# Kernel optimization log

Hardware: AMD Instinct MI355X
Metric: run time of the kernel (lower is better)

## Reference

```python
import jax, jax.numpy as jnp
import numpy as np

B, S, H = 16, 1024, 1024  # S must equal H for the original bmm to type-check


def setup_inputs() -> dict:
    key = jax.random.key(0)
    k1, k2, k3, k4, k5 = jax.random.split(key, 5)
    ht = jax.random.normal(k1, (B, H), dtype=jnp.float32)
    encoder_out = jax.random.normal(k2, (B, S, H), dtype=jnp.float32)
    # nn.Linear(2H, H): weight [H, 2H], bias [H]
    W_attn = jax.random.normal(k3, (H, 2 * H), dtype=jnp.float32) / np.sqrt(2 * H)
    b_attn = jax.random.normal(k4, (H,), dtype=jnp.float32) * 0.01
    # nn.Linear(H, 1, bias=False): weight [1, H]  (computed in forward but its output is discarded)
    W_v = jax.random.normal(k5, (1, H), dtype=jnp.float32) / np.sqrt(H)
    return {"ht": ht, "encoder_out": encoder_out, "W_attn": W_attn, "b_attn": b_attn, "W_v": W_v}


def reference(ht, encoder_out, W_attn, b_attn, W_v):
    b, s, h = encoder_out.shape
    # ht.repeat(S,1,1).transpose(0,1) -> [B,S,H]
    ht_rep = jnp.broadcast_to(ht[:, None, :], (b, s, h))
    energy = jnp.concatenate([ht_rep, encoder_out], axis=2)          # [B,S,2H]
    energy = jnp.tanh(jnp.einsum('bsk,hk->bsh', energy, W_attn) + b_attn)  # [B,S,H]
    # v projection is computed in the original forward but not returned (dead output)
    _attention = jnp.einsum('bsh,oh->bso', energy, W_v)[..., 0]      # [B,S], unused
    # NOTE: softmax over dim=1 (the seq axis) of the full 3D energy, as in the original
    attention_weights = jax.nn.softmax(energy, axis=1)               # [B,S,H]
    # bmm([B,S,H],[B,S,H]) with S==H: contract weights' H axis vs encoder_out's S axis
    context = jnp.einsum('bsk,bkh->bsh', attention_weights, encoder_out)  # [B,S,H]
    return (context, attention_weights)
```

## Files before the change

kernel.cpp:

```cpp
#include <hip/hip_runtime.h>
#include <math.h>

#define Bn 16
#define Sn 1024
#define Hn 1024
static const size_t SH = (size_t)Sn * Hn;
static const size_t BSH = (size_t)Bn * Sn * Hn;

typedef __attribute__((ext_vector_type(8))) short short8;
typedef __attribute__((ext_vector_type(4))) float f32x4;

#define GLD16(gp, lp) __builtin_amdgcn_global_load_lds( \
    (const __attribute__((address_space(1))) void*)(gp), \
    (__attribute__((address_space(3))) void*)(lp), 16, 0, 0)

__device__ __forceinline__ short bfr(float f) {
  union { float f; unsigned u; } v; v.f = f;
  unsigned r = (v.u + 0x7FFFu + ((v.u >> 16) & 1u)) >> 16;
  return (short)r;
}
__device__ __forceinline__ float b2f(unsigned short u) {
  union { unsigned u; float f; } v; v.u = (unsigned)u << 16; return v.f;
}
__device__ __forceinline__ short8 cvt8(float4 x, float4 y) {
  short8 r;
  r[0] = bfr(x.x); r[1] = bfr(x.y); r[2] = bfr(x.z); r[3] = bfr(x.w);
  r[4] = bfr(y.x); r[5] = bfr(y.y); r[6] = bfr(y.z); r[7] = bfr(y.w);
  return r;
}

__device__ __forceinline__ int swz8(int row, int g) {
  return (g & ~7) | ((g & 7) ^ (row & 7));
}

__global__ __launch_bounds__(256) void fused_cvt_kernel(const float* __restrict__ enc,
                                                        short* __restrict__ enc_bf,
                                                        short* __restrict__ encT) {
  __shared__ float tile[64][65];
  const int b = blockIdx.z;
  const int s0 = blockIdx.y * 64, h0 = blockIdx.x * 64;
  const int t = threadIdx.x;
  const int tr = t >> 4, tc = t & 15;
  const float* src = enc + (size_t)b * SH;
#pragma unroll
  for (int i = 0; i < 4; ++i) {
    const int s = i * 16 + tr;
    const float4 v = *(const float4*)(src + (size_t)(s0 + s) * 1024 + h0 + tc * 4);
    tile[s][tc * 4 + 0] = v.x; tile[s][tc * 4 + 1] = v.y;
    tile[s][tc * 4 + 2] = v.z; tile[s][tc * 4 + 3] = v.w;
  }
  __syncthreads();
  {
    const int rloc = t >> 2;
    const int rg = b * 1024 + s0 + rloc;
#pragma unroll
    for (int jj = 0; jj < 2; ++jj) {
      const int jloc = (t & 3) * 2 + jj;
      const int slot = jloc ^ (rg & 7);
      const float4 x = *(const float4*)&tile[rloc][jloc * 8];
      const float4 y = *(const float4*)&tile[rloc][jloc * 8 + 4];
      *(short8*)(enc_bf + (size_t)rg * 1024 + h0 + slot * 8) = cvt8(x, y);
    }
  }
  {
    const int hr = t >> 2, cs = t & 3;
    const int h = h0 + hr;
#pragma unroll
    for (int blk = 0; blk < 2; ++blk) {
      const int sg = blk * 4 + cs;
      const int gl = (s0 >> 3) + sg;
      const int gst = swz8(h, gl);
      short8 pk;
#pragma unroll
      for (int j = 0; j < 8; ++j) pk[j] = bfr(tile[sg * 8 + j][hr]);
      *(short8*)(encT + (size_t)b * SH + (size_t)h * 1024 + gst * 8) = pk;
    }
  }
}

__global__ __launch_bounds__(256) void cvt_enc_kernel(const float* __restrict__ enc,
                                                      short* __restrict__ enc_bf) {
  const int g = blockIdx.x * 256 + threadIdx.x;
  const int row = g >> 7;
  const int cs = g & 127;
  const float4 x = *(const float4*)(enc + (size_t)row * 1024 + cs * 8);
  const float4 y = *(const float4*)(enc + (size_t)row * 1024 + cs * 8 + 4);
  *(short8*)(enc_bf + (size_t)row * 1024 + swz8(row, cs) * 8) = cvt8(x, y);
}

__global__ __launch_bounds__(256) void cvt_w2_kernel(const float* __restrict__ W_attn,
                                                     short* __restrict__ W2_bf) {
  const int g = blockIdx.x * 256 + threadIdx.x;
  const int h = g >> 7;
  const int cs = g & 127;
  const float4 x = *(const float4*)(W_attn + (size_t)h * 2048 + 1024 + cs * 8);
  const float4 y = *(const float4*)(W_attn + (size_t)h * 2048 + 1024 + cs * 8 + 4);
  *(short8*)(W2_bf + (size_t)h * 1024 + swz8(h, cs) * 8) = cvt8(x, y);
}

__global__ __launch_bounds__(256) void c1_kernel(const float* __restrict__ ht,
                                                 const float* __restrict__ W_attn,
                                                 const float* __restrict__ b_attn,
                                                 float* __restrict__ c1) {
  __shared__ float hts[16384];
  const int t = threadIdx.x;
#pragma unroll
  for (int i = 0; i < 16; ++i)
    *(float4*)&hts[i * 1024 + t * 4] = *(const float4*)&ht[i * 1024 + t * 4];
  __syncthreads();
  const int h = blockIdx.x * 4 + (t >> 6);
  const int lane = t & 63;
  const float* w = W_attn + (size_t)h * 2048;
  float s[16];
#pragma unroll
  for (int b = 0; b < 16; ++b) s[b] = 0.f;
  for (int k = lane; k < 1024; k += 64) {
    const float wv = w[k];
#pragma unroll
    for (int b = 0; b < 16; ++b) s[b] = fmaf(wv, hts[b * 1024 + k], s[b]);
  }
#pragma unroll
  for (int b = 0; b < 16; ++b) {
    float v = s[b];
#pragma unroll
    for (int off = 32; off; off >>= 1) v += __shfl_down(v, off, 64);
    if (lane == 0) c1[b * 1024 + h] = v + b_attn[h];
  }
}

__global__ __launch_bounds__(256) void energy_mfma5(const short* __restrict__ enc_bf,
                                                    const short* __restrict__ W2_bf,
                                                    const float* __restrict__ c1,
                                                    short* __restrict__ Xbf,
                                                    float* __restrict__ colsum) {
  __shared__ __align__(16) short SMEM[2 * 128 * 64];
  short* Ast = SMEM;
  short* Bst = SMEM + 128 * 64;
  const int flat = blockIdx.x + (blockIdx.y << 3) + (blockIdx.z << 6);
  const int swz = (flat & 7) * 128 + (flat >> 3);
  const int b = swz >> 6;
  const int row0 = ((swz >> 3) & 7) * 128;
  const int col0 = (swz & 7) * 128;
  const int t = threadIdx.x;
  const int l = t & 63;
  const int w = t >> 6;
  const int wr = w >> 1, wc = w & 1;
  const int fr = l & 15, kg = l >> 4;

  const short* Abase = enc_bf + (size_t)b * SH + (size_t)(row0 + w * 32 + (l >> 3)) * 1024 + (l & 7) * 8;
  const short* Bbase = W2_bf + (size_t)(col0 + w * 32 + (l >> 3)) * 1024 + (l & 7) * 8;
  short* Alds = Ast + w * 2048;
  short* Blds = Bst + w * 2048;

  f32x4 acc[4][4] = {};

  for (int k0 = 0; k0 < 1024; k0 += 64) {
#pragma unroll
    for (int j = 0; j < 4; ++j) {
      GLD16(Abase + k0 + j * 8 * 1024, Alds + j * 512);
      GLD16(Bbase + k0 + j * 8 * 1024, Blds + j * 512);
    }
    __syncthreads();
#pragma unroll
    for (int kk = 0; kk < 2; ++kk) {
      short8 af[4], bf4[4];
#pragma unroll
      for (int m = 0; m < 4; ++m) {
        const int r = wr * 64 + m * 16 + fr;
        af[m] = *(const short8*)&Ast[r * 64 + (((kk * 4 + kg) ^ (r & 7)) << 3)];
      }
#pragma unroll
      for (int n = 0; n < 4; ++n) {
        const int r = wc * 64 + n * 16 + fr;
        bf4[n] = *(const short8*)&Bst[r * 64 + (((kk * 4 + kg) ^ (r & 7)) << 3)];
      }
#pragma unroll
      for (int m = 0; m < 4; ++m)
#pragma unroll
        for (int n = 0; n < 4; ++n)
          acc[m][n] = __builtin_amdgcn_mfma_f32_16x16x32_bf16(af[m], bf4[n], acc[m][n], 0, 0, 0);
    }
    __syncthreads();
  }

  unsigned short* obuf = (unsigned short*)SMEM;
#pragma unroll
  for (int n = 0; n < 4; ++n) {
    const int col_loc = wc * 64 + n * 16 + fr;
    const float c1v = c1[b * 1024 + col0 + col_loc];
    float csum = 0.f;
#pragma unroll
    for (int m = 0; m < 4; ++m) {
      const int rbase = wr * 64 + m * 16 + kg * 4;
#pragma unroll
      for (int r = 0; r < 4; ++r) {
        const float x = acc[m][n][r] + c1v;
        const float e = __expf(2.f * x);
        const float X = __expf((e - 1.f) / (e + 1.f));
        csum += X;
        const int row = rbase + r;
        obuf[row * 128 + (col_loc ^ ((row & 7) << 3))] = (unsigned short)bfr(X);
      }
    }
    csum += __shfl_xor(csum, 16);
    csum += __shfl_xor(csum, 32);
    if (l < 16) atomicAdd(&colsum[b * 1024 + col0 + col_loc], csum);
  }
  __syncthreads();
  const int orow = t >> 1;
  short* gdst = Xbf + (size_t)b * SH + (size_t)(row0 + orow) * 1024 + col0;
#pragma unroll
  for (int j = 0; j < 8; ++j) {
    const int slot = (t & 1) * 8 + j;
    *(short8*)(gdst + slot * 8) = *(short8*)&obuf[orow * 128 + slot * 8];
  }
}

__global__ __launch_bounds__(256) void rcp_kernel(const float* __restrict__ cs,
                                                  float* __restrict__ ci) {
  const int i = blockIdx.x * 256 + threadIdx.x;
  ci[i] = 1.0f / cs[i];
}

__global__ __launch_bounds__(256) void scale_v1(short* __restrict__ Xbf,
                                                const float* __restrict__ colinv,
                                                float* __restrict__ aw) {
  const size_t gid = (size_t)blockIdx.x * 256 + threadIdx.x;
  const int rg = (int)(gid >> 7);
  const int ss = (int)(gid & 127);
  const int b = rg >> 10;
  const int gl = (ss & ~7) | ((ss & 7) ^ (rg & 7));
  const int h0 = gl * 8;
  short* p = Xbf + (size_t)rg * 1024 + ss * 8;
  const short8 v = *(const short8*)p;
  const float4 ci0 = *(const float4*)(colinv + (b << 10) + h0);
  const float4 ci1 = *(const float4*)(colinv + (b << 10) + h0 + 4);
  float f[8];
  f[0] = b2f((unsigned short)v[0]) * ci0.x; f[1] = b2f((unsigned short)v[1]) * ci0.y;
  f[2] = b2f((unsigned short)v[2]) * ci0.z; f[3] = b2f((unsigned short)v[3]) * ci0.w;
  f[4] = b2f((unsigned short)v[4]) * ci1.x; f[5] = b2f((unsigned short)v[5]) * ci1.y;
  f[6] = b2f((unsigned short)v[6]) * ci1.z; f[7] = b2f((unsigned short)v[7]) * ci1.w;
  float4 o0 = {f[0], f[1], f[2], f[3]};
  float4 o1 = {f[4], f[5], f[6], f[7]};
  *(float4*)(aw + (size_t)rg * 1024 + h0) = o0;
  *(float4*)(aw + (size_t)rg * 1024 + h0 + 4) = o1;
  short8 r;
#pragma unroll
  for (int j = 0; j < 8; ++j) r[j] = bfr(f[j]);
  *(short8*)p = r;
}

__global__ __launch_bounds__(256) void context_gld(const short* __restrict__ awbf,
                                                   const short* __restrict__ encT,
                                                   float* __restrict__ ctx) {
  __shared__ __align__(16) short Ast[128 * 64];
  __shared__ __align__(16) short Bst[128 * 64];
  const int flat = blockIdx.x + (blockIdx.y << 3) + (blockIdx.z << 6);
  const int swz = (flat & 7) * 128 + (flat >> 3);
  const int b = swz >> 6;
  const int row0 = ((swz >> 3) & 7) * 128;
  const int col0 = (swz & 7) * 128;
  const int t = threadIdx.x;
  const int l = t & 63;
  const int w = t >> 6;
  const int wr = w >> 1, wc = w & 1;
  const int fr = l & 15, kg = l >> 4;

  const short* Abase = awbf + (size_t)b * SH + (size_t)(row0 + w * 32 + (l >> 3)) * 1024 + (l & 7) * 8;
  const short* Bbase = encT + (size_t)b * SH + (size_t)(col0 + w * 32 + (l >> 3)) * 1024 + (l & 7) * 8;
  short* Alds = Ast + w * 2048;
  short* Blds = Bst + w * 2048;

  f32x4 acc[4][4] = {};

  for (int k0 = 0; k0 < 1024; k0 += 64) {
#pragma unroll
    for (int j = 0; j < 4; ++j) {
      GLD16(Abase + k0 + j * 8 * 1024, Alds + j * 512);
      GLD16(Bbase + k0 + j * 8 * 1024, Blds + j * 512);
    }
    __syncthreads();
#pragma unroll
    for (int kk = 0; kk < 2; ++kk) {
      short8 af[4], bf4[4];
#pragma unroll
      for (int m = 0; m < 4; ++m) {
        const int r = wr * 64 + m * 16 + fr;
        af[m] = *(const short8*)&Ast[r * 64 + (((kk * 4 + kg) ^ (r & 7)) << 3)];
      }
#pragma unroll
      for (int n = 0; n < 4; ++n) {
        const int r = wc * 64 + n * 16 + fr;
        bf4[n] = *(const short8*)&Bst[r * 64 + (((kk * 4 + kg) ^ (r & 7)) << 3)];
      }
#pragma unroll
      for (int m = 0; m < 4; ++m)
#pragma unroll
        for (int n = 0; n < 4; ++n)
          acc[m][n] = __builtin_amdgcn_mfma_f32_16x16x32_bf16(af[m], bf4[n], acc[m][n], 0, 0, 0);
    }
    __syncthreads();
  }

  float* Cb = ctx + (size_t)b * SH;
#pragma unroll
  for (int n = 0; n < 4; ++n) {
    const int col = col0 + wc * 64 + n * 16 + fr;
#pragma unroll
    for (int m = 0; m < 4; ++m) {
      const int r0 = row0 + wr * 64 + m * 16 + kg * 4;
#pragma unroll
      for (int r = 0; r < 4; ++r)
        Cb[(size_t)(r0 + r) * 1024 + col] = acc[m][n][r];
    }
  }
}

__global__ __launch_bounds__(256) void energy_mfma4(const short* __restrict__ enc_bf,
                                                    const short* __restrict__ W2_bf,
                                                    const float* __restrict__ c1,
                                                    float* __restrict__ X) {
  __shared__ __align__(16) short Ast[128 * 64];
  __shared__ __align__(16) short Bst[128 * 64];
  const int flat = blockIdx.x + (blockIdx.y << 3) + (blockIdx.z << 6);
  const int swz = (flat & 7) * 128 + (flat >> 3);
  const int b = swz >> 6;
  const int row0 = ((swz >> 3) & 7) * 128;
  const int col0 = (swz & 7) * 128;
  const int t = threadIdx.x;
  const int l = t & 63;
  const int w = t >> 6;
  const int wr = w >> 1, wc = w & 1;
  const int fr = l & 15, kg = l >> 4;

  const short* Abase = enc_bf + (size_t)b * SH + (size_t)(row0 + w * 32 + (l >> 3)) * 1024 + (l & 7) * 8;
  const short* Bbase = W2_bf + (size_t)(col0 + w * 32 + (l >> 3)) * 1024 + (l & 7) * 8;
  short* Alds = Ast + w * 2048;
  short* Blds = Bst + w * 2048;

  f32x4 acc[4][4] = {};

  for (int k0 = 0; k0 < 1024; k0 += 64) {
#pragma unroll
    for (int j = 0; j < 4; ++j) {
      GLD16(Abase + k0 + j * 8 * 1024, Alds + j * 512);
      GLD16(Bbase + k0 + j * 8 * 1024, Blds + j * 512);
    }
    __syncthreads();
#pragma unroll
    for (int kk = 0; kk < 2; ++kk) {
      short8 af[4], bf4[4];
#pragma unroll
      for (int m = 0; m < 4; ++m) {
        const int r = wr * 64 + m * 16 + fr;
        af[m] = *(const short8*)&Ast[r * 64 + (((kk * 4 + kg) ^ (r & 7)) << 3)];
      }
#pragma unroll
      for (int n = 0; n < 4; ++n) {
        const int r = wc * 64 + n * 16 + fr;
        bf4[n] = *(const short8*)&Bst[r * 64 + (((kk * 4 + kg) ^ (r & 7)) << 3)];
      }
#pragma unroll
      for (int m = 0; m < 4; ++m)
#pragma unroll
        for (int n = 0; n < 4; ++n)
          acc[m][n] = __builtin_amdgcn_mfma_f32_16x16x32_bf16(af[m], bf4[n], acc[m][n], 0, 0, 0);
    }
    __syncthreads();
  }

  float* Xb = X + (size_t)b * SH;
#pragma unroll
  for (int n = 0; n < 4; ++n) {
    const int col = col0 + wc * 64 + n * 16 + fr;
    const float c1v = c1[b * 1024 + col];
#pragma unroll
    for (int m = 0; m < 4; ++m) {
      const int r0 = row0 + wr * 64 + m * 16 + kg * 4;
#pragma unroll
      for (int r = 0; r < 4; ++r) {
        const float x = acc[m][n][r] + c1v;
        const float e = __expf(2.f * x);
        Xb[(size_t)(r0 + r) * 1024 + col] = __expf((e - 1.f) / (e + 1.f));
      }
    }
  }
}

__global__ __launch_bounds__(256) void norm_kernel(float* __restrict__ X) {
  const int b = blockIdx.x >> 4;
  const int hg = blockIdx.x & 15;
  const int l = threadIdx.x & 63;
  const int sg = threadIdx.x >> 6;
  float* col = X + (size_t)b * SH + hg * 64 + l;
  const int s0 = sg * 256;
  float sum = 0.f;
#pragma unroll 8
  for (int s = s0; s < s0 + 256; ++s) sum += col[(size_t)s * 1024];
  __shared__ float red[4][64];
  red[sg][l] = sum;
  __syncthreads();
  const float inv = 1.f / (red[0][l] + red[1][l] + red[2][l] + red[3][l]);
#pragma unroll 8
  for (int s = s0; s < s0 + 256; ++s) col[(size_t)s * 1024] *= inv;
}

__global__ __launch_bounds__(256) void context_fast(const float* __restrict__ aw,
                                                    const short* __restrict__ encT,
                                                    float* __restrict__ ctx) {
  __shared__ __align__(16) short Ast[128 * 64];
  __shared__ __align__(16) short Bst[128 * 64];
  const int flat = blockIdx.x + (blockIdx.y << 3) + (blockIdx.z << 6);
  const int swz = (flat & 7) * 128 + (flat >> 3);
  const int b = swz >> 6;
  const int row0 = ((swz >> 3) & 7) * 128;
  const int col0 = (swz & 7) * 128;
  const int t = threadIdx.x;
  const int l = t & 63;
  const int w = t >> 6;
  const int wr = w >> 1, wc = w & 1;
  const int fr = l & 15, kg = l >> 4;

  const int sr = t >> 1;
  const int gc0 = (t & 1) * 4;
  const float* arow = aw + (size_t)b * SH + (size_t)(row0 + sr) * 1024;
  const short* Bbase = encT + (size_t)b * SH + (size_t)(col0 + w * 32 + (l >> 3)) * 1024 + (l & 7) * 8;
  short* Blds = Bst + w * 2048;

  float4 pa[8];
#pragma unroll
  for (int j = 0; j < 4; ++j) {
    pa[2 * j]     = *(const float4*)(arow + (gc0 + j) * 8);
    pa[2 * j + 1] = *(const float4*)(arow + (gc0 + j) * 8 + 4);
  }

  f32x4 acc[4][4] = {};

  for (int k0 = 0; k0 < 1024; k0 += 64) {
#pragma unroll
    for (int j = 0; j < 4; ++j)
      GLD16(Bbase + k0 + j * 8 * 1024, Blds + j * 512);
#pragma unroll
    for (int j = 0; j < 4; ++j)
      *(short8*)&Ast[sr * 64 + (((gc0 + j) ^ (sr & 7)) << 3)] = cvt8(pa[2 * j], pa[2 * j + 1]);
    if (k0 != 960) {
#pragma unroll
      for (int j = 0; j < 4; ++j) {
        pa[2 * j]     = *(const float4*)(arow + k0 + 64 + (gc0 + j) * 8);
        pa[2 * j + 1] = *(const float4*)(arow + k0 + 64 + (gc0 + j) * 8 + 4);
      }
    }
    __syncthreads();
#pragma unroll
    for (int kk = 0; kk < 2; ++kk) {
      short8 af[4], bf4[4];
#pragma unroll
      for (int m = 0; m < 4; ++m) {
        const int r = wr * 64 + m * 16 + fr;
        af[m] = *(const short8*)&Ast[r * 64 + (((kk * 4 + kg) ^ (r & 7)) << 3)];
      }
#pragma unroll
      for (int n = 0; n < 4; ++n) {
        const int r = wc * 64 + n * 16 + fr;
        bf4[n] = *(const short8*)&Bst[r * 64 + (((kk * 4 + kg) ^ (r & 7)) << 3)];
      }
#pragma unroll
      for (int m = 0; m < 4; ++m)
#pragma unroll
        for (int n = 0; n < 4; ++n)
          acc[m][n] = __builtin_amdgcn_mfma_f32_16x16x32_bf16(af[m], bf4[n], acc[m][n], 0, 0, 0);
    }
    __syncthreads();
  }

  float* Cb = ctx + (size_t)b * SH;
#pragma unroll
  for (int n = 0; n < 4; ++n) {
    const int col = col0 + wc * 64 + n * 16 + fr;
#pragma unroll
    for (int m = 0; m < 4; ++m) {
      const int r0 = row0 + wr * 64 + m * 16 + kg * 4;
#pragma unroll
      for (int r = 0; r < 4; ++r)
        Cb[(size_t)(r0 + r) * 1024 + col] = acc[m][n][r];
    }
  }
}

__global__ __launch_bounds__(256) void context_mfma(const float* __restrict__ aw,
                                                    const float* __restrict__ enc,
                                                    float* __restrict__ ctx) {
  __shared__ __align__(16) short Ast[128 * 32];
  __shared__ __align__(16) short Bst[128 * 32];
  const int b = blockIdx.z;
  const int row0 = blockIdx.y * 128;
  const int col0 = blockIdx.x * 128;
  const int t = threadIdx.x;
  const int l = t & 63;
  const int w = t >> 6;
  const int wr = w >> 1, wc = w & 1;
  const int fr = l & 15, kg = l >> 4;

  const int sr = t >> 1;
  const int sc0 = (t & 1) * 2;
  const float* arow = aw + (size_t)b * SH + (size_t)(row0 + sr) * 1024;
  const int bcol = t & 127;
  const int kb0 = (t >> 7) * 2;
  const float* bcolp = enc + (size_t)b * SH + col0 + bcol;

  f32x4 acc[4][4] = {};

  for (int k0 = 0; k0 < 1024; k0 += 32) {
    const float4 a0 = *(const float4*)(arow + k0 + sc0 * 8);
    const float4 a1 = *(const float4*)(arow + k0 + sc0 * 8 + 4);
    const float4 a2 = *(const float4*)(arow + k0 + sc0 * 8 + 8);
    const float4 a3 = *(const float4*)(arow + k0 + sc0 * 8 + 12);
    float bv[2][8];
#pragma unroll
    for (int j = 0; j < 2; ++j)
#pragma unroll
      for (int i = 0; i < 8; ++i)
        bv[j][i] = bcolp[(size_t)(k0 + (kb0 + j) * 8 + i) * 1024];
    __syncthreads();
    *(short8*)&Ast[sr * 32 + ((sc0 ^ ((sr >> 1) & 3)) << 3)]       = cvt8(a0, a1);
    *(short8*)&Ast[sr * 32 + (((sc0 + 1) ^ ((sr >> 1) & 3)) << 3)] = cvt8(a2, a3);
#pragma unroll
    for (int j = 0; j < 2; ++j) {
      short8 pk;
#pragma unroll
      for (int i = 0; i < 8; ++i) pk[i] = bfr(bv[j][i]);
      *(short8*)&Bst[bcol * 32 + (((kb0 + j) ^ ((bcol >> 1) & 3)) << 3)] = pk;
    }
    __syncthreads();
    short8 af[4], bf4[4];
#pragma unroll
    for (int m = 0; m < 4; ++m) {
      const int r = wr * 64 + m * 16 + fr;
      af[m] = *(const short8*)&Ast[r * 32 + ((kg ^ ((r >> 1) & 3)) << 3)];
    }
#pragma unroll
    for (int n = 0; n < 4; ++n) {
      const int r = wc * 64 + n * 16 + fr;
      bf4[n] = *(const short8*)&Bst[r * 32 + ((kg ^ ((r >> 1) & 3)) << 3)];
    }
#pragma unroll
    for (int m = 0; m < 4; ++m)
#pragma unroll
      for (int n = 0; n < 4; ++n)
        acc[m][n] = __builtin_amdgcn_mfma_f32_16x16x32_bf16(af[m], bf4[n], acc[m][n], 0, 0, 0);
  }

  float* Cb = ctx + (size_t)b * SH;
#pragma unroll
  for (int n = 0; n < 4; ++n) {
    const int col = col0 + wc * 64 + n * 16 + fr;
#pragma unroll
    for (int m = 0; m < 4; ++m) {
      const int r0 = row0 + wr * 64 + m * 16 + kg * 4;
#pragma unroll
      for (int r = 0; r < 4; ++r)
        Cb[(size_t)(r0 + r) * 1024 + col] = acc[m][n][r];
    }
  }
}

extern "C" void kernel_launch(void* const* d_in, const int* in_sizes, int n_in,
                              void* d_out, int out_size, void* d_ws, size_t ws_size,
                              hipStream_t stream) {
  (void)in_sizes; (void)n_in; (void)out_size;
  const float* ht     = (const float*)d_in[0];
  const float* enc    = (const float*)d_in[1];
  const float* W_attn = (const float*)d_in[2];
  const float* b_attn = (const float*)d_in[3];

  float* ctx = (float*)d_out;
  float* aw  = ctx + BSH;

  short* enc_bf = (short*)ctx;
  short* W2_bf  = (short*)(ctx + 8388608);
  float* c1f    = ctx + 8912896;
  float* colsum = c1f + 16384;
  float* colinv = c1f + 32768;

  const bool ws1 = ws_size >= ((size_t)32 << 20);
  const bool ws2 = ws_size >= ((size_t)64 << 20);
  short* encT = (short*)d_ws;
  short* Xbf  = (short*)((char*)d_ws + ((size_t)32 << 20));

  cvt_w2_kernel<<<512, 256, 0, stream>>>(W_attn, W2_bf);
  c1_kernel<<<Hn / 4, 256, 0, stream>>>(ht, W_attn, b_attn, c1f);

  if (ws1) {
    dim3 gt(16, 16, Bn);
    fused_cvt_kernel<<<gt, 256, 0, stream>>>(enc, enc_bf, encT);
  } else {
    cvt_enc_kernel<<<8192, 256, 0, stream>>>(enc, enc_bf);
  }

  dim3 g(8, 8, Bn);
  if (ws2) {
    hipMemsetAsync(colsum, 0, 65536, stream);
    energy_mfma5<<<g, 256, 0, stream>>>(enc_bf, W2_bf, c1f, Xbf, colsum);
    rcp_kernel<<<64, 256, 0, stream>>>(colsum, colinv);
    scale_v1<<<8192, 256, 0, stream>>>(Xbf, colinv, aw);
    context_gld<<<g, 256, 0, stream>>>(Xbf, encT, ctx);
  } else {
    energy_mfma4<<<g, 256, 0, stream>>>(enc_bf, W2_bf, c1f, aw);
    norm_kernel<<<Bn * 16, 256, 0, stream>>>(aw);
    if (ws1)
      context_fast<<<g, 256, 0, stream>>>(aw, encT, ctx);
    else
      context_mfma<<<g, 256, 0, stream>>>(aw, enc, ctx);
  }
}
```

Measured before the change: 180.4 us.

## Replace direct global-to-LDS loads with register-prefetched K=32 tiles in GEMM kernels

Drops the global_load_lds path and the swizzled global layouts of the bf16 buffers. The GEMM kernels now stage 32-wide K slices in registers, prefetch the next slice, and write them to LDS with an XOR swizzle, halving LDS per block. The Xbf swizzle moves into the energy epilogue's LDS read, and scale_v1 indexing is simplified to match. The intent is better overlap of global loads with MFMA work and higher occupancy, at the cost of twice as many barriers per K and register-staged copies.

```diff
diff --git a/kernel.cpp b/kernel.cpp
--- a/kernel.cpp
+++ b/kernel.cpp
@@ -10,10 +10,6 @@
 typedef __attribute__((ext_vector_type(8))) short short8;
 typedef __attribute__((ext_vector_type(4))) float f32x4;
 
-#define GLD16(gp, lp) __builtin_amdgcn_global_load_lds( \
-    (const __attribute__((address_space(1))) void*)(gp), \
-    (__attribute__((address_space(3))) void*)(lp), 16, 0, 0)
-
 __device__ __forceinline__ short bfr(float f) {
   union { float f; unsigned u; } v; v.f = f;
   unsigned r = (v.u + 0x7FFFu + ((v.u >> 16) & 1u)) >> 16;
@@ -27,10 +23,6 @@
   r[0] = bfr(x.x); r[1] = bfr(x.y); r[2] = bfr(x.z); r[3] = bfr(x.w);
   r[4] = bfr(y.x); r[5] = bfr(y.y); r[6] = bfr(y.z); r[7] = bfr(y.w);
   return r;
-}
-
-__device__ __forceinline__ int swz8(int row, int g) {
-  return (g & ~7) | ((g & 7) ^ (row & 7));
 }
 
 __global__ __launch_bounds__(256) void fused_cvt_kernel(const float* __restrict__ enc,
@@ -56,10 +48,9 @@
 #pragma unroll
     for (int jj = 0; jj < 2; ++jj) {
       const int jloc = (t & 3) * 2 + jj;
-      const int slot = jloc ^ (rg & 7);
       const float4 x = *(const float4*)&tile[rloc][jloc * 8];
       const float4 y = *(const float4*)&tile[rloc][jloc * 8 + 4];
-      *(short8*)(enc_bf + (size_t)rg * 1024 + h0 + slot * 8) = cvt8(x, y);
+      *(short8*)(enc_bf + (size_t)rg * 1024 + h0 + jloc * 8) = cvt8(x, y);
     }
   }
   {
@@ -69,11 +60,10 @@
     for (int blk = 0; blk < 2; ++blk) {
       const int sg = blk * 4 + cs;
       const int gl = (s0 >> 3) + sg;
-      const int gst = swz8(h, gl);
       short8 pk;
 #pragma unroll
       for (int j = 0; j < 8; ++j) pk[j] = bfr(tile[sg * 8 + j][hr]);
-      *(short8*)(encT + (size_t)b * SH + (size_t)h * 1024 + gst * 8) = pk;
+      *(short8*)(encT + (size_t)b * SH + (size_t)h * 1024 + gl * 8) = pk;
     }
   }
 }
@@ -85,7 +75,7 @@
   const int cs = g & 127;
   const float4 x = *(const float4*)(enc + (size_t)row * 1024 + cs * 8);
   const float4 y = *(const float4*)(enc + (size_t)row * 1024 + cs * 8 + 4);
-  *(short8*)(enc_bf + (size_t)row * 1024 + swz8(row, cs) * 8) = cvt8(x, y);
+  *(short8*)(enc_bf + (size_t)row * 1024 + cs * 8) = cvt8(x, y);
 }
 
 __global__ __launch_bounds__(256) void cvt_w2_kernel(const float* __restrict__ W_attn,
@@ -95,7 +85,7 @@
   const int cs = g & 127;
   const float4 x = *(const float4*)(W_attn + (size_t)h * 2048 + 1024 + cs * 8);
   const float4 y = *(const float4*)(W_attn + (size_t)h * 2048 + 1024 + cs * 8 + 4);
-  *(short8*)(W2_bf + (size_t)h * 1024 + swz8(h, cs) * 8) = cvt8(x, y);
+  *(short8*)(W2_bf + (size_t)h * 1024 + cs * 8) = cvt8(x, y);
 }
 
 __global__ __launch_bounds__(256) void c1_kernel(const float* __restrict__ ht,
@@ -128,14 +118,16 @@
   }
 }
 
-__global__ __launch_bounds__(256) void energy_mfma5(const short* __restrict__ enc_bf,
-                                                    const short* __restrict__ W2_bf,
-                                                    const float* __restrict__ c1,
-                                                    short* __restrict__ Xbf,
-                                                    float* __restrict__ colsum) {
-  __shared__ __align__(16) short SMEM[2 * 128 * 64];
-  short* Ast = SMEM;
-  short* Bst = SMEM + 128 * 64;
+#define LSLOT(r, g) ((r) * 32 + (((g) ^ (((r) >> 1) & 3)) << 3))
+
+__global__ __launch_bounds__(256) void energy_v2(const short* __restrict__ enc_bf,
+                                                 const short* __restrict__ W2_bf,
+                                                 const float* __restrict__ c1,
+                                                 short* __restrict__ Xbf,
+                                                 float* __restrict__ colsum) {
+  __shared__ __align__(16) short SM[16384];
+  short* Ast = SM;
+  short* Bst = SM + 4096;
   const int flat = blockIdx.x + (blockIdx.y << 3) + (blockIdx.z << 6);
   const int swz = (flat & 7) * 128 + (flat >> 3);
   const int b = swz >> 6;
@@ -147,43 +139,52 @@
   const int wr = w >> 1, wc = w & 1;
   const int fr = l & 15, kg = l >> 4;
 
-  const short* Abase = enc_bf + (size_t)b * SH + (size_t)(row0 + w * 32 + (l >> 3)) * 1024 + (l & 7) * 8;
-  const short* Bbase = W2_bf + (size_t)(col0 + w * 32 + (l >> 3)) * 1024 + (l & 7) * 8;
-  short* Alds = Ast + w * 2048;
-  short* Blds = Bst + w * 2048;
+  const int sr = t >> 1;
+  const int sc0 = (t & 1) * 2;
+  const short* aptr = enc_bf + (size_t)b * SH + (size_t)(row0 + sr) * 1024 + sc0 * 8;
+  const short* bptr = W2_bf + (size_t)(col0 + sr) * 1024 + sc0 * 8;
+  const int sl0 = LSLOT(sr, sc0);
+  const int sl1 = LSLOT(sr, sc0 + 1);
+
+  short8 pa0 = *(const short8*)(aptr);
+  short8 pa1 = *(const short8*)(aptr + 8);
+  short8 pb0 = *(const short8*)(bptr);
+  short8 pb1 = *(const short8*)(bptr + 8);
 
   f32x4 acc[4][4] = {};
 
-  for (int k0 = 0; k0 < 1024; k0 += 64) {
-#pragma unroll
-    for (int j = 0; j < 4; ++j) {
-      GLD16(Abase + k0 + j * 8 * 1024, Alds + j * 512);
-      GLD16(Bbase + k0 + j * 8 * 1024, Blds + j * 512);
-    }
-    __syncthreads();
-#pragma unroll
-    for (int kk = 0; kk < 2; ++kk) {
-      short8 af[4], bf4[4];
-#pragma unroll
-      for (int m = 0; m < 4; ++m) {
-        const int r = wr * 64 + m * 16 + fr;
-        af[m] = *(const short8*)&Ast[r * 64 + (((kk * 4 + kg) ^ (r & 7)) << 3)];
-      }
-#pragma unroll
-      for (int n = 0; n < 4; ++n) {
-        const int r = wc * 64 + n * 16 + fr;
-        bf4[n] = *(const short8*)&Bst[r * 64 + (((kk * 4 + kg) ^ (r & 7)) << 3)];
-      }
-#pragma unroll
-      for (int m = 0; m < 4; ++m)
-#pragma unroll
-        for (int n = 0; n < 4; ++n)
-          acc[m][n] = __builtin_amdgcn_mfma_f32_16x16x32_bf16(af[m], bf4[n], acc[m][n], 0, 0, 0);
-    }
-    __syncthreads();
-  }
-
-  unsigned short* obuf = (unsigned short*)SMEM;
+  for (int k0 = 0; k0 < 1024; k0 += 32) {
+    *(short8*)&Ast[sl0] = pa0;
+    *(short8*)&Ast[sl1] = pa1;
+    *(short8*)&Bst[sl0] = pb0;
+    *(short8*)&Bst[sl1] = pb1;
+    if (k0 != 992) {
+      pa0 = *(const short8*)(aptr + k0 + 32);
+      pa1 = *(const short8*)(aptr + k0 + 40);
+      pb0 = *(const short8*)(bptr + k0 + 32);
+      pb1 = *(const short8*)(bptr + k0 + 40);
+    }
+    __syncthreads();
+    short8 af[4], bf4[4];
+#pragma unroll
+    for (int m = 0; m < 4; ++m) {
+      const int r = wr * 64 + m * 16 + fr;
+      af[m] = *(const short8*)&Ast[LSLOT(r, kg)];
+    }
+#pragma unroll
+    for (int n = 0; n < 4; ++n) {
+      const int r = wc * 64 + n * 16 + fr;
+      bf4[n] = *(const short8*)&Bst[LSLOT(r, kg)];
+    }
+#pragma unroll
+    for (int m = 0; m < 4; ++m)
+#pragma unroll
+      for (int n = 0; n < 4; ++n)
+        acc[m][n] = __builtin_amdgcn_mfma_f32_16x16x32_bf16(af[m], bf4[n], acc[m][n], 0, 0, 0);
+    __syncthreads();
+  }
+
+  unsigned short* obuf = (unsigned short*)SM;
 #pragma unroll
   for (int n = 0; n < 4; ++n) {
     const int col_loc = wc * 64 + n * 16 + fr;
@@ -212,7 +213,7 @@
 #pragma unroll
   for (int j = 0; j < 8; ++j) {
     const int slot = (t & 1) * 8 + j;
-    *(short8*)(gdst + slot * 8) = *(short8*)&obuf[orow * 128 + slot * 8];
+    *(short8*)(gdst + slot * 8) = *(short8*)&obuf[orow * 128 + ((slot ^ (orow & 7)) << 3)];
   }
 }
 
@@ -227,11 +228,10 @@
                                                 float* __restrict__ aw) {
   const size_t gid = (size_t)blockIdx.x * 256 + threadIdx.x;
   const int rg = (int)(gid >> 7);
-  const int ss = (int)(gid & 127);
+  const int gl = (int)(gid & 127);
   const int b = rg >> 10;
-  const int gl = (ss & ~7) | ((ss & 7) ^ (rg & 7));
   const int h0 = gl * 8;
-  short* p = Xbf + (size_t)rg * 1024 + ss * 8;
+  short* p = Xbf + (size_t)rg * 1024 + h0;
   const short8 v = *(const short8*)p;
   const float4 ci0 = *(const float4*)(colinv + (b << 10) + h0);
   const float4 ci1 = *(const float4*)(colinv + (b << 10) + h0 + 4);
@@ -250,11 +250,12 @@
   *(short8*)p = r;
 }
 
-__global__ __launch_bounds__(256) void context_gld(const short* __restrict__ awbf,
-                                                   const short* __restrict__ encT,
-                                                   float* __restrict__ ctx) {
-  __shared__ __align__(16) short Ast[128 * 64];
-  __shared__ __align__(16) short Bst[128 * 64];
+__global__ __launch_bounds__(256) void context_v2(const short* __restrict__ awbf,
+                                                  const short* __restrict__ encT,
+                                                  float* __restrict__ ctx) {
+  __shared__ __align__(16) short SM[8192];
+  short* Ast = SM;
+  short* Bst = SM + 4096;
   const int flat = blockIdx.x + (blockIdx.y << 3) + (blockIdx.z << 6);
   const int swz = (flat & 7) * 128 + (flat >> 3);
   const int b = swz >> 6;
@@ -266,39 +267,48 @@
   const int wr = w >> 1, wc = w & 1;
   const int fr = l & 15, kg = l >> 4;
 
-  const short* Abase = awbf + (size_t)b * SH + (size_t)(row0 + w * 32 + (l >> 3)) * 1024 + (l & 7) * 8;
-  const short* Bbase = encT + (size_t)b * SH + (size_t)(col0 + w * 32 + (l >> 3)) * 1024 + (l & 7) * 8;
-  short* Alds = Ast + w * 2048;
-  short* Blds = Bst + w * 2048;
+  const int sr = t >> 1;
+  const int sc0 = (t & 1) * 2;
+  const short* aptr = awbf + (size_t)b * SH + (size_t)(row0 + sr) * 1024 + sc0 * 8;
+  const short* bptr = encT + (size_t)b * SH + (size_t)(col0 + sr) * 1024 + sc0 * 8;
+  const int sl0 = LSLOT(sr, sc0);
+  const int sl1 = LSLOT(sr, sc0 + 1);
+
+  short8 pa0 = *(const short8*)(aptr);
+  short8 pa1 = *(const short8*)(aptr + 8);
+  short8 pb0 = *(const short8*)(bptr);
+  short8 pb1 = *(const short8*)(bptr + 8);
 
   f32x4 acc[4][4] = {};
 
-  for (int k0 = 0; k0 < 1024; k0 += 64) {
-#pragma unroll
-    for (int j = 0; j < 4; ++j) {
-      GLD16(Abase + k0 + j * 8 * 1024, Alds + j * 512);
-      GLD16(Bbase + k0 + j * 8 * 1024, Blds + j * 512);
-    }
-    __syncthreads();
-#pragma unroll
-    for (int kk = 0; kk < 2; ++kk) {
-      short8 af[4], bf4[4];
-#pragma unroll
-      for (int m = 0; m < 4; ++m) {
-        const int r = wr * 64 + m * 16 + fr;
-        af[m] = *(const short8*)&Ast[r * 64 + (((kk * 4 + kg) ^ (r & 7)) << 3)];
-      }
-#pragma unroll
-      for (int n = 0; n < 4; ++n) {
-        const int r = wc * 64 + n * 16 + fr;
-        bf4[n] = *(const short8*)&Bst[r * 64 + (((kk * 4 + kg) ^ (r & 7)) << 3)];
-      }
-#pragma unroll
-      for (int m = 0; m < 4; ++m)
-#pragma unroll
-        for (int n = 0; n < 4; ++n)
-          acc[m][n] = __builtin_amdgcn_mfma_f32_16x16x32_bf16(af[m], bf4[n], acc[m][n], 0, 0, 0);
-    }
+  for (int k0 = 0; k0 < 1024; k0 += 32) {
+    *(short8*)&Ast[sl0] = pa0;
+    *(short8*)&Ast[sl1] = pa1;
+    *(short8*)&Bst[sl0] = pb0;
+    *(short8*)&Bst[sl1] = pb1;
+    if (k0 != 992) {
+      pa0 = *(const short8*)(aptr + k0 + 32);
+      pa1 = *(const short8*)(aptr + k0 + 40);
+      pb0 = *(const short8*)(bptr + k0 + 32);
+      pb1 = *(const short8*)(bptr + k0 + 40);
+    }
+    __syncthreads();
+    short8 af[4], bf4[4];
+#pragma unroll
+    for (int m = 0; m < 4; ++m) {
+      const int r = wr * 64 + m * 16 + fr;
+      af[m] = *(const short8*)&Ast[LSLOT(r, kg)];
+    }
+#pragma unroll
+    for (int n = 0; n < 4; ++n) {
+      const int r = wc * 64 + n * 16 + fr;
+      bf4[n] = *(const short8*)&Bst[LSLOT(r, kg)];
+    }
+#pragma unroll
+    for (int m = 0; m < 4; ++m)
+#pragma unroll
+      for (int n = 0; n < 4; ++n)
+        acc[m][n] = __builtin_amdgcn_mfma_f32_16x16x32_bf16(af[m], bf4[n], acc[m][n], 0, 0, 0);
     __syncthreads();
   }
 
@@ -316,12 +326,13 @@
   }
 }
 
-__global__ __launch_bounds__(256) void energy_mfma4(const short* __restrict__ enc_bf,
-                                                    const short* __restrict__ W2_bf,
-                                                    const float* __restrict__ c1,
-                                                    float* __restrict__ X) {
-  __shared__ __align__(16) short Ast[128 * 64];
-  __shared__ __align__(16) short Bst[128 * 64];
+__global__ __launch_bounds__(256) void energy_v2f(const short* __restrict__ enc_bf,
+                                                  const short* __restrict__ W2_bf,
+                                                  const float* __restrict__ c1,
+                                                  float* __restrict__ X) {
+  __shared__ __align__(16) short SM[8192];
+  short* Ast = SM;
+  short* Bst = SM + 4096;
   const int flat = blockIdx.x + (blockIdx.y << 3) + (blockIdx.z << 6);
   const int swz = (flat & 7) * 128 + (flat >> 3);
   const int b = swz >> 6;
@@ -333,39 +344,48 @@
   const int wr = w >> 1, wc = w & 1;
   const int fr = l & 15, kg = l >> 4;
 
-  const short* Abase = enc_bf + (size_t)b * SH + (size_t)(row0 + w * 32 + (l >> 3)) * 1024 + (l & 7) * 8;
-  const short* Bbase = W2_bf + (size_t)(col0 + w * 32 + (l >> 3)) * 1024 + (l & 7) * 8;
-  short* Alds = Ast + w * 2048;
-  short* Blds = Bst + w * 2048;
+  const int sr = t >> 1;
+  const int sc0 = (t & 1) * 2;
+  const short* aptr = enc_bf + (size_t)b * SH + (size_t)(row0 + sr) * 1024 + sc0 * 8;
+  const short* bptr = W2_bf + (size_t)(col0 + sr) * 1024 + sc0 * 8;
+  const int sl0 = LSLOT(sr, sc0);
+  const int sl1 = LSLOT(sr, sc0 + 1);
+
+  short8 pa0 = *(const short8*)(aptr);
+  short8 pa1 = *(const short8*)(aptr + 8);
+  short8 pb0 = *(const short8*)(bptr);
+  short8 pb1 = *(const short8*)(bptr + 8);
 
   f32x4 acc[4][4] = {};
 
-  for (int k0 = 0; k0 < 1024; k0 += 64) {
-#pragma unroll
-    for (int j = 0; j < 4; ++j) {
-      GLD16(Abase + k0 + j * 8 * 1024, Alds + j * 512);
-      GLD16(Bbase + k0 + j * 8 * 1024, Blds + j * 512);
-    }
-    __syncthreads();
-#pragma unroll
-    for (int kk = 0; kk < 2; ++kk) {
-      short8 af[4], bf4[4];
-#pragma unroll
-      for (int m = 0; m < 4; ++m) {
-        const int r = wr * 64 + m * 16 + fr;
-        af[m] = *(const short8*)&Ast[r * 64 + (((kk * 4 + kg) ^ (r & 7)) << 3)];
-      }
-#pragma unroll
-      for (int n = 0; n < 4; ++n) {
-        const int r = wc * 64 + n * 16 + fr;
-        bf4[n] = *(const short8*)&Bst[r * 64 + (((kk * 4 + kg) ^ (r & 7)) << 3)];
-      }
-#pragma unroll
-      for (int m = 0; m < 4; ++m)
-#pragma unroll
-        for (int n = 0; n < 4; ++n)
-          acc[m][n] = __builtin_amdgcn_mfma_f32_16x16x32_bf16(af[m], bf4[n], acc[m][n], 0, 0, 0);
-    }
+  for (int k0 = 0; k0 < 1024; k0 += 32) {
+    *(short8*)&Ast[sl0] = pa0;
+    *(short8*)&Ast[sl1] = pa1;
+    *(short8*)&Bst[sl0] = pb0;
+    *(short8*)&Bst[sl1] = pb1;
+    if (k0 != 992) {
+      pa0 = *(const short8*)(aptr + k0 + 32);
+      pa1 = *(const short8*)(aptr + k0 + 40);
+      pb0 = *(const short8*)(bptr + k0 + 32);
+      pb1 = *(const short8*)(bptr + k0 + 40);
+    }
+    __syncthreads();
+    short8 af[4], bf4[4];
+#pragma unroll
+    for (int m = 0; m < 4; ++m) {
+      const int r = wr * 64 + m * 16 + fr;
+      af[m] = *(const short8*)&Ast[LSLOT(r, kg)];
+    }
+#pragma unroll
+    for (int n = 0; n < 4; ++n) {
+      const int r = wc * 64 + n * 16 + fr;
+      bf4[n] = *(const short8*)&Bst[LSLOT(r, kg)];
+    }
+#pragma unroll
+    for (int m = 0; m < 4; ++m)
+#pragma unroll
+      for (int n = 0; n < 4; ++n)
+        acc[m][n] = __builtin_amdgcn_mfma_f32_16x16x32_bf16(af[m], bf4[n], acc[m][n], 0, 0, 0);
     __syncthreads();
   }
 
@@ -405,11 +425,12 @@
   for (int s = s0; s < s0 + 256; ++s) col[(size_t)s * 1024] *= inv;
 }
 
-__global__ __launch_bounds__(256) void context_fast(const float* __restrict__ aw,
-                                                    const short* __restrict__ encT,
-                                                    float* __restrict__ ctx) {
-  __shared__ __align__(16) short Ast[128 * 64];
-  __shared__ __align__(16) short Bst[128 * 64];
+__global__ __launch_bounds__(256) void context_fast2(const float* __restrict__ aw,
+                                                     const short* __restrict__ encT,
+                                                     float* __restrict__ ctx) {
+  __shared__ __align__(16) short SM[8192];
+  short* Ast = SM;
+  short* Bst = SM + 4096;
   const int flat = blockIdx.x + (blockIdx.y << 3) + (blockIdx.z << 6);
   const int swz = (flat & 7) * 128 + (flat >> 3);
   const int b = swz >> 6;
@@ -422,54 +443,51 @@
   const int fr = l & 15, kg = l >> 4;
 
   const int sr = t >> 1;
-  const int gc0 = (t & 1) * 4;
-  const float* arow = aw + (size_t)b * SH + (size_t)(row0 + sr) * 1024;
-  const short* Bbase = encT + (size_t)b * SH + (size_t)(col0 + w * 32 + (l >> 3)) * 1024 + (l & 7) * 8;
-  short* Blds = Bst + w * 2048;
-
-  float4 pa[8];
-#pragma unroll
-  for (int j = 0; j < 4; ++j) {
-    pa[2 * j]     = *(const float4*)(arow + (gc0 + j) * 8);
-    pa[2 * j + 1] = *(const float4*)(arow + (gc0 + j) * 8 + 4);
-  }
+  const int sc0 = (t & 1) * 2;
+  const float* aptr = aw + (size_t)b * SH + (size_t)(row0 + sr) * 1024 + sc0 * 8;
+  const short* bptr = encT + (size_t)b * SH + (size_t)(col0 + sr) * 1024 + sc0 * 8;
+  const int sl0 = LSLOT(sr, sc0);
+  const int sl1 = LSLOT(sr, sc0 + 1);
+
+  float4 fa0 = *(const float4*)(aptr);
+  float4 fa1 = *(const float4*)(aptr + 4);
+  float4 fa2 = *(const float4*)(aptr + 8);
+  float4 fa3 = *(const float4*)(aptr + 12);
+  short8 pb0 = *(const short8*)(bptr);
+  short8 pb1 = *(const short8*)(bptr + 8);
 
   f32x4 acc[4][4] = {};
 
-  for (int k0 = 0; k0 < 1024; k0 += 64) {
-#pragma unroll
-    for (int j = 0; j < 4; ++j)
-      GLD16(Bbase + k0 + j * 8 * 1024, Blds + j * 512);
-#pragma unroll
-    for (int j = 0; j < 4; ++j)
-      *(short8*)&Ast[sr * 64 + (((gc0 + j) ^ (sr & 7)) << 3)] = cvt8(pa[2 * j], pa[2 * j + 1]);
-    if (k0 != 960) {
-#pragma unroll
-      for (int j = 0; j < 4; ++j) {
-        pa[2 * j]     = *(const float4*)(arow + k0 + 64 + (gc0 + j) * 8);
-        pa[2 * j + 1] = *(const float4*)(arow + k0 + 64 + (gc0 + j) * 8 + 4);
-      }
-    }
-    __syncthreads();
-#pragma unroll
-    for (int kk = 0; kk < 2; ++kk) {
-      short8 af[4], bf4[4];
-#pragma unroll
-      for (int m = 0; m < 4; ++m) {
-        const int r = wr * 64 + m * 16 + fr;
-        af[m] = *(const short8*)&Ast[r * 64 + (((kk * 4 + kg) ^ (r & 7)) << 3)];
-      }
-#pragma unroll
-      for (int n = 0; n < 4; ++n) {
-        const int r = wc * 64 + n * 16 + fr;
-        bf4[n] = *(const short8*)&Bst[r * 64 + (((kk * 4 + kg) ^ (r & 7)) << 3)];
-      }
-#pragma unroll
-      for (int m = 0; m < 4; ++m)
-#pragma unroll
-        for (int n = 0; n < 4; ++n)
-          acc[m][n] = __builtin_amdgcn_mfma_f32_16x16x32_bf16(af[m], bf4[n], acc[m][n], 0, 0, 0);
-    }
+  for (int k0 = 0; k0 < 1024; k0 += 32) {
+    *(short8*)&Ast[sl0] = cvt8(fa0, fa1);
+    *(short8*)&Ast[sl1] = cvt8(fa2, fa3);
+    *(short8*)&Bst[sl0] = pb0;
+    *(short8*)&Bst[sl1] = pb1;
+    if (k0 != 992) {
+      fa0 = *(const float4*)(aptr + k0 + 32);
+      fa1 = *(const float4*)(aptr + k0 + 36);
+      fa2 = *(const float4*)(aptr + k0 + 40);
+      fa3 = *(const float4*)(aptr + k0 + 44);
+      pb0 = *(const short8*)(bptr + k0 + 32);
+      pb1 = *(const short8*)(bptr + k0 + 40);
+    }
+    __syncthreads();
+    short8 af[4], bf4[4];
+#pragma unroll
+    for (int m = 0; m < 4; ++m) {
+      const int r = wr * 64 + m * 16 + fr;
+      af[m] = *(const short8*)&Ast[LSLOT(r, kg)];
+    }
+#pragma unroll
+    for (int n = 0; n < 4; ++n) {
+      const int r = wc * 64 + n * 16 + fr;
+      bf4[n] = *(const short8*)&Bst[LSLOT(r, kg)];
+    }
+#pragma unroll
+    for (int m = 0; m < 4; ++m)
+#pragma unroll
+      for (int n = 0; n < 4; ++n)
+        acc[m][n] = __builtin_amdgcn_mfma_f32_16x16x32_bf16(af[m], bf4[n], acc[m][n], 0, 0, 0);
     __syncthreads();
   }
 
@@ -522,26 +540,26 @@
       for (int i = 0; i < 8; ++i)
         bv[j][i] = bcolp[(size_t)(k0 + (kb0 + j) * 8 + i) * 1024];
     __syncthreads();
-    *(short8*)&Ast[sr * 32 + ((sc0 ^ ((sr >> 1) & 3)) << 3)]       = cvt8(a0, a1);
-    *(short8*)&Ast[sr * 32 + (((sc0 + 1) ^ ((sr >> 1) & 3)) << 3)] = cvt8(a2, a3);
+    *(short8*)&Ast[LSLOT(sr, sc0)]     = cvt8(a0, a1);
+    *(short8*)&Ast[LSLOT(sr, sc0 + 1)] = cvt8(a2, a3);
 #pragma unroll
     for (int j = 0; j < 2; ++j) {
       short8 pk;
 #pragma unroll
       for (int i = 0; i < 8; ++i) pk[i] = bfr(bv[j][i]);
-      *(short8*)&Bst[bcol * 32 + (((kb0 + j) ^ ((bcol >> 1) & 3)) << 3)] = pk;
+      *(short8*)&Bst[LSLOT(bcol, kb0 + j)] = pk;
     }
     __syncthreads();
     short8 af[4], bf4[4];
 #pragma unroll
     for (int m = 0; m < 4; ++m) {
       const int r = wr * 64 + m * 16 + fr;
-      af[m] = *(const short8*)&Ast[r * 32 + ((kg ^ ((r >> 1) & 3)) << 3)];
+      af[m] = *(const short8*)&Ast[LSLOT(r, kg)];
     }
 #pragma unroll
     for (int n = 0; n < 4; ++n) {
       const int r = wc * 64 + n * 16 + fr;
-      bf4[n] = *(const short8*)&Bst[r * 32 + ((kg ^ ((r >> 1) & 3)) << 3)];
+      bf4[n] = *(const short8*)&Bst[LSLOT(r, kg)];
     }
 #pragma unroll
     for (int m = 0; m < 4; ++m)
@@ -600,15 +618,15 @@
   dim3 g(8, 8, Bn);
   if (ws2) {
     hipMemsetAsync(colsum, 0, 65536, stream);
-    energy_mfma5<<<g, 256, 0, stream>>>(enc_bf, W2_bf, c1f, Xbf, colsum);
+    energy_v2<<<g, 256, 0, stream>>>(enc_bf, W2_bf, c1f, Xbf, colsum);
     rcp_kernel<<<64, 256, 0, stream>>>(colsum, colinv);
     scale_v1<<<8192, 256, 0, stream>>>(Xbf, colinv, aw);
-    context_gld<<<g, 256, 0, stream>>>(Xbf, encT, ctx);
+    context_v2<<<g, 256, 0, stream>>>(Xbf, encT, ctx);
   } else {
-    energy_mfma4<<<g, 256, 0, stream>>>(enc_bf, W2_bf, c1f, aw);
+    energy_v2f<<<g, 256, 0, stream>>>(enc_bf, W2_bf, c1f, aw);
     norm_kernel<<<Bn * 16, 256, 0, stream>>>(aw);
     if (ws1)
-      context_fast<<<g, 256, 0, stream>>>(aw, encT, ctx);
+      context_fast2<<<g, 256, 0, stream>>>(aw, encT, ctx);
     else
       context_mfma<<<g, 256, 0, stream>>>(aw, enc, ctx);
   }
```

Measured after the change: 190.1 us. +5.4%, slower.
